# Kernel tuning notes

Measured on AMD Instinct MI355X. Metric: run time of the kernel, lower is better.

## Reference

```python
import jax, jax.numpy as jnp
import numpy as np

NUM_BINS = 256
HIST_MIN = -1.0
HIST_MAX = 1.0
EPS = 1e-8


def _histc(x, bins=NUM_BINS, lo=HIST_MIN, hi=HIST_MAX):
    # Faithful to torch.histc: values outside [lo, hi] are ignored;
    # value == hi falls into the last bin.
    x = x.reshape(-1)
    width = (hi - lo) / bins
    idx = jnp.clip(jnp.floor((x - lo) / width).astype(jnp.int32), 0, bins - 1)
    in_range = ((x >= lo) & (x <= hi)).astype(jnp.float32)
    return jax.ops.segment_sum(in_range, idx, num_segments=bins)


def _entropy(hist):
    prob = hist / jnp.sum(hist) + EPS
    return -jnp.sum(prob * jnp.log(prob))


def setup_inputs() -> dict:
    key = jax.random.key(0)
    k1, k2 = jax.random.split(key)
    shape = (64, 2, 512, 512)
    predicted_ab = jax.random.normal(k1, shape, dtype=jnp.float32)
    ground_truth_ab = jax.random.normal(k2, shape, dtype=jnp.float32)
    return {"predicted_ab": predicted_ab, "ground_truth_ab": ground_truth_ab}


def reference(predicted_ab, ground_truth_ab):
    pred_hist = _histc(predicted_ab)
    gt_hist = _histc(ground_truth_ab)
    return jnp.abs(_entropy(pred_hist) - _entropy(gt_hist))
```

## Files before the change

### kernel.cpp

```cpp
#include <hip/hip_runtime.h>
#include <math.h>

#define NBINS 256
#define TRASH 255

__global__ __launch_bounds__(64) void hist2_kernel(const float* __restrict__ a,
                                                   const float* __restrict__ b,
                                                   unsigned int* __restrict__ ghist,
                                                   int n4a, int n4b, int na, int nb,
                                                   int half_blocks) {
#pragma clang fp contract(off)
    __shared__ unsigned short lh[NBINS * 64];
    const int lane = threadIdx.x;

    uint4* z = (uint4*)lh;
#pragma unroll
    for (int k = 0; k < 32; k++) z[lane + 64 * k] = make_uint4(0u, 0u, 0u, 0u);
    __syncthreads();

    const int which = (blockIdx.x >= half_blocks) ? 1 : 0;
    const float4* __restrict__ x4 = (const float4*)(which ? b : a);
    const float* __restrict__ x1 = which ? b : a;
    const int n4 = which ? n4b : n4a;
    const int n = which ? nb : na;
    const int bid = which ? (blockIdx.x - half_blocks) : blockIdx.x;
    const int stride = half_blocks * 64;
    unsigned int r255 = 0;

#define ROWOF(f, rowv)                                            \
    {                                                             \
        float _u = ((f) + 1.0f) * 128.0f;                         \
        int _bi = (int)_u;                                        \
        _bi = _bi > 255 ? 255 : _bi;                              \
        bool _in = ((f) >= -1.0f) & ((f) <= 1.0f);                \
        r255 += (_in & (_bi == 255)) ? 1u : 0u;                   \
        rowv = _in ? _bi : TRASH;                                 \
    }

#define BATCH4(v)                                                                 \
    {                                                                             \
        int r0, r1, r2, r3;                                                       \
        ROWOF((v).x, r0) ROWOF((v).y, r1) ROWOF((v).z, r2) ROWOF((v).w, r3)       \
        int e01 = (r1 == r0), e02 = (r2 == r0), e12 = (r2 == r1);                 \
        int e03 = (r3 == r0), e13 = (r3 == r1), e23 = (r3 == r2);                 \
        int c0 = 1 + e01 + e02 + e03;                                             \
        int c1 = 1 + e12 + e13;                                                   \
        int c2 = 1 + e23;                                                         \
        int w1 = e01 ? TRASH : r1;                                                \
        int w2 = (e02 | e12) ? TRASH : r2;                                        \
        int w3 = (e03 | e13 | e23) ? TRASH : r3;                                  \
        int i0 = (r0 << 6) | lane, i1 = (w1 << 6) | lane;                         \
        int i2 = (w2 << 6) | lane, i3 = (w3 << 6) | lane;                         \
        unsigned short v0 = lh[i0], v1 = lh[i1], v2 = lh[i2], v3 = lh[i3];        \
        lh[i0] = (unsigned short)(v0 + c0);                                       \
        lh[i1] = (unsigned short)(v1 + c1);                                       \
        lh[i2] = (unsigned short)(v2 + c2);                                       \
        lh[i3] = (unsigned short)(v3 + 1);                                        \
    }

    int i = bid * 64 + lane;
    for (; i + 7 * stride < n4; i += 8 * stride) {
        float4 v0 = x4[i];
        float4 v1 = x4[i + stride];
        float4 v2 = x4[i + 2 * stride];
        float4 v3 = x4[i + 3 * stride];
        float4 v4 = x4[i + 4 * stride];
        float4 v5 = x4[i + 5 * stride];
        float4 v6 = x4[i + 6 * stride];
        float4 v7 = x4[i + 7 * stride];
        BATCH4(v0) BATCH4(v1) BATCH4(v2) BATCH4(v3)
        BATCH4(v4) BATCH4(v5) BATCH4(v6) BATCH4(v7)
    }
    for (; i < n4; i += stride) {
        float4 v = x4[i];
        BATCH4(v)
    }
    for (int t = n4 * 4 + bid * 64 + lane; t < n; t += stride) {
        int r;
        ROWOF(x1[t], r)
        int idx = (r << 6) | lane;
        lh[idx] = (unsigned short)(lh[idx] + 1);
    }

    __syncthreads();

    const unsigned int* lhd = (const unsigned int*)lh;
#pragma unroll
    for (int k = 0; k < 4; k++) {
        const int bin = lane + (k << 6);
        if (bin < 255) {
            unsigned int lo = 0, hi = 0;
#pragma unroll
            for (int jj = 0; jj < 32; jj++) {
                const int j = (jj + lane) & 31;
                const unsigned int v = lhd[(bin << 5) + j];
                lo += v & 0xFFFFu;
                hi += v >> 16;
            }
            atomicAdd(&ghist[(which << 8) + bin], lo + hi);
        }
    }
    unsigned int s = r255;
#pragma unroll
    for (int o = 32; o > 0; o >>= 1) s += __shfl_down(s, o, 64);
    if (lane == 0 && s) atomicAdd(&ghist[(which << 8) + 255], s);
}

__global__ __launch_bounds__(256) void entropy_kernel(const unsigned int* __restrict__ gh,
                                                      float* __restrict__ out) {
    __shared__ double sd[NBINS];
    const int tid = threadIdx.x;
    double e[2];

    for (int h = 0; h < 2; h++) {
        const double hv = (double)gh[h * NBINS + tid];

        sd[tid] = hv;
        __syncthreads();
        for (int o = 128; o > 0; o >>= 1) {
            if (tid < o) sd[tid] += sd[tid + o];
            __syncthreads();
        }
        const double total = sd[0];
        __syncthreads();

        const double p = hv / total + 1e-8;
        sd[tid] = -p * log(p);
        __syncthreads();
        for (int o = 128; o > 0; o >>= 1) {
            if (tid < o) sd[tid] += sd[tid + o];
            __syncthreads();
        }
        e[h] = sd[0];
        __syncthreads();
    }

    if (tid == 0) out[0] = (float)fabs(e[0] - e[1]);
}

extern "C" void kernel_launch(void* const* d_in, const int* in_sizes, int n_in,
                              void* d_out, int out_size, void* d_ws, size_t ws_size,
                              hipStream_t stream) {
    const float* pred = (const float*)d_in[0];
    const float* gt   = (const float*)d_in[1];
    const int n0 = in_sizes[0];
    const int n1 = in_sizes[1];

    unsigned int* hist = (unsigned int*)d_ws;
    hipMemsetAsync(d_ws, 0, 2 * NBINS * sizeof(unsigned int), stream);

    const int half_blocks = 640;
    hist2_kernel<<<2 * half_blocks, 64, 0, stream>>>(pred, gt, hist,
                                                     n0 / 4, n1 / 4, n0, n1,
                                                     half_blocks);
    entropy_kernel<<<1, 256, 0, stream>>>(hist, (float*)d_out);
}
```

Before: 334.5 us.

## Shrink per-lane LDS histogram to 8-bit counters and prefetch-pipeline loads

Per-lane shared-memory counters go from 16-bit to 8-bit, with two bins interleaved per 16-bit pair. This halves LDS per block to 16 KB, which allows more resident blocks. The float4 load loop is software-pipelined so the next 8 vectors are loaded while the current ones are binned, and the grid is doubled. The reduction unpacks byte pairs with masked adds. The risk is 8-bit overflow if many elements per lane land in one bin, which is safe only because each lane processes a limited number of elements.

After: 417.0 us. +24.6%, slower.

```diff
diff --git a/kernel.cpp b/kernel.cpp
--- a/kernel.cpp
+++ b/kernel.cpp
@@ -10,12 +10,12 @@
                                                    int n4a, int n4b, int na, int nb,
                                                    int half_blocks) {
 #pragma clang fp contract(off)
-    __shared__ unsigned short lh[NBINS * 64];
+    __shared__ unsigned char lh[NBINS * 64];
     const int lane = threadIdx.x;
 
     uint4* z = (uint4*)lh;
 #pragma unroll
-    for (int k = 0; k < 32; k++) z[lane + 64 * k] = make_uint4(0u, 0u, 0u, 0u);
+    for (int k = 0; k < 16; k++) z[lane + 64 * k] = make_uint4(0u, 0u, 0u, 0u);
     __syncthreads();
 
     const int which = (blockIdx.x >= half_blocks) ? 1 : 0;
@@ -26,6 +26,8 @@
     const int bid = which ? (blockIdx.x - half_blocks) : blockIdx.x;
     const int stride = half_blocks * 64;
     unsigned int r255 = 0;
+
+#define IDXOF(row) ((((row) >> 1) << 7) | (lane << 1) | ((row) & 1))
 
 #define ROWOF(f, rowv)                                            \
     {                                                             \
@@ -49,56 +51,62 @@
         int w1 = e01 ? TRASH : r1;                                                \
         int w2 = (e02 | e12) ? TRASH : r2;                                        \
         int w3 = (e03 | e13 | e23) ? TRASH : r3;                                  \
-        int i0 = (r0 << 6) | lane, i1 = (w1 << 6) | lane;                         \
-        int i2 = (w2 << 6) | lane, i3 = (w3 << 6) | lane;                         \
-        unsigned short v0 = lh[i0], v1 = lh[i1], v2 = lh[i2], v3 = lh[i3];        \
-        lh[i0] = (unsigned short)(v0 + c0);                                       \
-        lh[i1] = (unsigned short)(v1 + c1);                                       \
-        lh[i2] = (unsigned short)(v2 + c2);                                       \
-        lh[i3] = (unsigned short)(v3 + 1);                                        \
+        int i0 = IDXOF(r0), i1 = IDXOF(w1), i2 = IDXOF(w2), i3 = IDXOF(w3);       \
+        unsigned char v0 = lh[i0], v1 = lh[i1], v2 = lh[i2], v3 = lh[i3];         \
+        lh[i0] = (unsigned char)(v0 + c0);                                        \
+        lh[i1] = (unsigned char)(v1 + c1);                                        \
+        lh[i2] = (unsigned char)(v2 + c2);                                        \
+        lh[i3] = (unsigned char)(v3 + 1);                                         \
     }
 
     int i = bid * 64 + lane;
-    for (; i + 7 * stride < n4; i += 8 * stride) {
-        float4 v0 = x4[i];
-        float4 v1 = x4[i + stride];
-        float4 v2 = x4[i + 2 * stride];
-        float4 v3 = x4[i + 3 * stride];
-        float4 v4 = x4[i + 4 * stride];
-        float4 v5 = x4[i + 5 * stride];
-        float4 v6 = x4[i + 6 * stride];
-        float4 v7 = x4[i + 7 * stride];
-        BATCH4(v0) BATCH4(v1) BATCH4(v2) BATCH4(v3)
-        BATCH4(v4) BATCH4(v5) BATCH4(v6) BATCH4(v7)
+    float4 r[8];
+#pragma unroll
+    for (int k = 0; k < 8; k++) {
+        int p = i + k * stride;
+        r[k] = x4[p < n4 ? p : (n4 - 1)];
     }
-    for (; i < n4; i += stride) {
-        float4 v = x4[i];
+    for (; i + 15 * stride < n4; i += 8 * stride) {
+#pragma unroll
+        for (int k = 0; k < 8; k++) {
+            float4 cur = r[k];
+            r[k] = x4[i + (k + 8) * stride];
+            BATCH4(cur)
+        }
+    }
+#pragma unroll
+    for (int k = 0; k < 8; k++) {
+        if (i + k * stride < n4) BATCH4(r[k])
+    }
+    for (int j = i + 8 * stride; j < n4; j += stride) {
+        float4 v = x4[j];
         BATCH4(v)
     }
     for (int t = n4 * 4 + bid * 64 + lane; t < n; t += stride) {
-        int r;
-        ROWOF(x1[t], r)
-        int idx = (r << 6) | lane;
-        lh[idx] = (unsigned short)(lh[idx] + 1);
+        int rr;
+        ROWOF(x1[t], rr)
+        int idx = IDXOF(rr);
+        lh[idx] = (unsigned char)(lh[idx] + 1);
     }
 
     __syncthreads();
 
     const unsigned int* lhd = (const unsigned int*)lh;
 #pragma unroll
-    for (int k = 0; k < 4; k++) {
-        const int bin = lane + (k << 6);
-        if (bin < 255) {
-            unsigned int lo = 0, hi = 0;
+    for (int k = 0; k < 2; k++) {
+        const int blk = 2 * lane + k;
+        unsigned int se = 0, so = 0;
 #pragma unroll
-            for (int jj = 0; jj < 32; jj++) {
-                const int j = (jj + lane) & 31;
-                const unsigned int v = lhd[(bin << 5) + j];
-                lo += v & 0xFFFFu;
-                hi += v >> 16;
-            }
-            atomicAdd(&ghist[(which << 8) + bin], lo + hi);
+        for (int jj = 0; jj < 32; jj++) {
+            const int j = (jj + lane) & 31;
+            const unsigned int v = lhd[(blk << 5) + j];
+            se += v & 0x00FF00FFu;
+            so += (v >> 8) & 0x00FF00FFu;
         }
+        const int rowE = 2 * blk, rowO = 2 * blk + 1;
+        atomicAdd(&ghist[(which << 8) + rowE], (se & 0xFFFFu) + (se >> 16));
+        if (rowO != TRASH)
+            atomicAdd(&ghist[(which << 8) + rowO], (so & 0xFFFFu) + (so >> 16));
     }
     unsigned int s = r255;
 #pragma unroll
@@ -149,7 +157,7 @@
     unsigned int* hist = (unsigned int*)d_ws;
     hipMemsetAsync(d_ws, 0, 2 * NBINS * sizeof(unsigned int), stream);
 
-    const int half_blocks = 640;
+    const int half_blocks = 1280;
     hist2_kernel<<<2 * half_blocks, 64, 0, stream>>>(pred, gt, hist,
                                                      n0 / 4, n1 / 4, n0, n1,
                                                      half_blocks);
```
